# Kernel tuning notes

Measured on AMD Instinct MI355X. Metric: run time of the kernel, lower is better.

## Reference

```python
import jax, jax.numpy as jnp
import numpy as np
import math

# Static multi-level spatial layout (H, W) per level and flattened start offsets.
SHAPES = ((100, 100), (50, 50), (25, 25), (13, 13))
STARTS = (0, 10000, 12500, 13125)
LEN_IN = 13294
D_MODEL, N_LEVELS, N_HEADS, N_POINTS = 256, 4, 8, 4
D_HEAD = D_MODEL // N_HEADS
B, LQ = 2, 13294


def _offset_bias():
    # Replicates MSDeformAttn._reset_parameters radial grid init for sampling_offsets.bias
    thetas = np.arange(N_HEADS, dtype=np.float32) * (2.0 * math.pi / N_HEADS)
    grid = np.stack([np.cos(thetas), np.sin(thetas)], axis=-1)  # [nh, 2]
    grid = grid / np.abs(grid).max(axis=-1, keepdims=True)
    # [nh, nl, np, 2] with per-point radius (i+1)
    full = np.tile(grid[:, None, None, :], (1, N_LEVELS, N_POINTS, 1))
    full = full * np.arange(1, N_POINTS + 1, dtype=np.float32)[None, None, :, None]
    return full.reshape(-1)


def setup_inputs() -> dict:
    key = jax.random.key(0)
    ks = jax.random.split(key, 8)
    xavier = 1.0 / math.sqrt(D_MODEL)
    return {
        "query": jax.random.normal(ks[0], (B, LQ, D_MODEL), jnp.float32),
        "reference_points": jax.random.uniform(ks[1], (B, LQ, N_LEVELS, 2), jnp.float32),
        "input_flatten": jax.random.normal(ks[2], (B, LEN_IN, D_MODEL), jnp.float32),
        "input_spatial_shapes": jnp.array(SHAPES, jnp.int32),
        "input_level_start_index": jnp.array(STARTS, jnp.int32),
        "W_off": jax.random.normal(ks[3], (D_MODEL, N_HEADS * N_LEVELS * N_POINTS * 2), jnp.float32) * 0.01,
        "b_off": jnp.asarray(_offset_bias()),
        "W_attn": jax.random.normal(ks[4], (D_MODEL, N_HEADS * N_LEVELS * N_POINTS), jnp.float32) * 0.02,
        "b_attn": jnp.zeros((N_HEADS * N_LEVELS * N_POINTS,), jnp.float32),
        "W_val": jax.random.normal(ks[5], (D_MODEL, D_MODEL), jnp.float32) * xavier,
        "b_val": jnp.zeros((D_MODEL,), jnp.float32),
        "W_out": jax.random.normal(ks[6], (D_MODEL, D_MODEL), jnp.float32) * xavier,
        "b_out": jnp.zeros((D_MODEL,), jnp.float32),
    }


def reference(query, reference_points, input_flatten, input_spatial_shapes,
              input_level_start_index, W_off, b_off, W_attn, b_attn,
              W_val, b_val, W_out, b_out):
    Bq, Lq, _ = query.shape
    value = (input_flatten @ W_val + b_val).reshape(Bq, LEN_IN, N_HEADS, D_HEAD)

    off = (query @ W_off + b_off).reshape(Bq, Lq, N_HEADS, N_LEVELS, N_POINTS, 2)
    aw = (query @ W_attn + b_attn).reshape(Bq, Lq, N_HEADS, N_LEVELS * N_POINTS)
    aw = jax.nn.softmax(aw, axis=-1).reshape(Bq, Lq, N_HEADS, N_LEVELS, N_POINTS)

    # offset normalizer is (W, H) per level
    normalizer = jnp.array([[w, h] for (h, w) in SHAPES], query.dtype)  # [nl, 2]
    loc = reference_points[:, :, None, :, None, :] + off / normalizer[None, None, None, :, None, :]

    bi = jnp.arange(Bq)[:, None, None, None]
    hi = jnp.arange(N_HEADS)[None, None, :, None]
    out = jnp.zeros((Bq, Lq, N_HEADS, D_HEAD), query.dtype)

    # Per-level zero-padded bilinear sampling (math-equivalent to grid_sample
    # align_corners=False, padding_mode='zeros' on the padded max_H x max_W grid,
    # since the padded region is zero-filled).
    for lvl, (H, W) in enumerate(SHAPES):
        s = STARTS[lvl]
        vflat = value[:, s:s + H * W]  # [B, H*W, nh, dh]
        l = loc[:, :, :, lvl]          # [B, Lq, nh, P, 2] in normalized coords
        x = l[..., 0] * W - 0.5
        y = l[..., 1] * H - 0.5
        x0 = jnp.floor(x)
        y0 = jnp.floor(y)
        sampled = jnp.zeros((Bq, Lq, N_HEADS, N_POINTS, D_HEAD), query.dtype)
        for dx in (0, 1):
            for dy in (0, 1):
                xi = x0 + dx
                yi = y0 + dy
                wgt = (1.0 - jnp.abs(x - xi)) * (1.0 - jnp.abs(y - yi))
                valid = (xi >= 0) & (xi <= W - 1) & (yi >= 0) & (yi <= H - 1)
                idx = (jnp.clip(yi, 0, H - 1) * W + jnp.clip(xi, 0, W - 1)).astype(jnp.int32)
                v = vflat[bi, idx, hi]  # [B, Lq, nh, P, dh]
                sampled = sampled + v * (wgt * valid)[..., None]
        out = out + jnp.einsum('bqhpd,bqhp->bqhd', sampled, aw[:, :, :, lvl])

    out = out.reshape(Bq, Lq, D_MODEL)
    return out @ W_out + b_out
```

## Files before the change

kernel.cpp:

```cpp
#include <hip/hip_runtime.h>
#include <math.h>

#define BQ 2
#define LQ 13294
#define LEN_IN 13294
#define D_MODEL 256
#define N_HEADS 8
#define N_LEVELS 4
#define N_POINTS 4
#define D_HEAD 32
#define M_ROWS (BQ * LQ)

__device__ __constant__ int c_HW[N_LEVELS]    = {100, 50, 25, 13};
__device__ __constant__ int c_START[N_LEVELS] = {0, 10000, 12500, 13125};

typedef __attribute__((ext_vector_type(8))) short bf16x8;
typedef __attribute__((ext_vector_type(4))) float f32x4;

__device__ inline unsigned short f2bf(float f) {
  union { float f; unsigned int u; } x; x.f = f;
  unsigned int u = x.u;
  unsigned int r = (u + 0x7fffu + ((u >> 16) & 1u)) >> 16;
  return (unsigned short)r;
}
__device__ inline float bf2f(unsigned short b) {
  union { unsigned int u; float f; } x; x.u = ((unsigned int)b) << 16;
  return x.f;
}

__global__ __launch_bounds__(256) void prep_weights(
    const float* __restrict__ W_off, const float* __restrict__ b_off,
    const float* __restrict__ W_attn, const float* __restrict__ b_attn,
    const float* __restrict__ W_val, const float* __restrict__ W_out,
    unsigned short* __restrict__ Wval_t, unsigned short* __restrict__ Woa_t,
    unsigned short* __restrict__ Wout_t, float* __restrict__ b_oa) {
  const int idx = blockIdx.x * 256 + threadIdx.x;
  const int SZ1 = 256 * 256;
  const int SZ2 = 384 * 256;
  if (idx < SZ1) {
    const int n = idx >> 8, k = idx & 255;
    Wval_t[idx] = f2bf(W_val[k * 256 + n]);
  } else if (idx < SZ1 + SZ2) {
    const int j = idx - SZ1;
    const int n = j >> 8, k = j & 255;
    const float v = (n < 256) ? W_off[k * 256 + n] : W_attn[k * 128 + (n - 256)];
    Woa_t[j] = f2bf(v);
  } else if (idx < SZ1 + SZ2 + SZ1) {
    const int j = idx - SZ1 - SZ2;
    const int n = j >> 8, k = j & 255;
    Wout_t[j] = f2bf(W_out[k * 256 + n]);
  }
  if (blockIdx.x == 0) b_oa[threadIdx.x] = b_off[threadIdx.x];
  if (blockIdx.x == 1 && threadIdx.x < 128)
    b_oa[256 + threadIdx.x] = b_attn[threadIdx.x];
}

#define BM 128
#define BN 128
#define BK 32
#define LDK 40

template <bool A_BF16, bool C_BF16>
__global__ __launch_bounds__(256) void gemm_mfma(
    const void* __restrict__ Ap, const unsigned short* __restrict__ Wt,
    const float* __restrict__ bias, void* __restrict__ Cp,
    int M, int N, int K) {
  __shared__ unsigned short As[BM * LDK];
  __shared__ unsigned short Bs[BN * LDK];
  const int tid = threadIdx.x;
  const int m0 = blockIdx.x * BM;
  const int n0 = blockIdx.y * BN;
  const int wave = tid >> 6;
  const int lane = tid & 63;
  const int wm = (wave & 1) * 64;
  const int wn = (wave >> 1) * 64;
  const int fr = lane & 15;
  const int fq = lane >> 4;

  f32x4 acc[4][4];
#pragma unroll
  for (int i = 0; i < 4; ++i)
#pragma unroll
    for (int j = 0; j < 4; ++j) acc[i][j] = (f32x4){0.f, 0.f, 0.f, 0.f};

  for (int k0 = 0; k0 < K; k0 += BK) {
    if (A_BF16) {
      const int m = tid >> 2;
      const int ch = tid & 3;
#pragma unroll
      for (int half = 0; half < 2; ++half) {
        const int mm = m + half * 64;
        const int gm = m0 + mm;
        uint4 v = make_uint4(0u, 0u, 0u, 0u);
        if (gm < M)
          v = *(const uint4*)((const unsigned short*)Ap + (size_t)gm * K + k0 + ch * 8);
        *(uint4*)&As[mm * LDK + ch * 8] = v;
      }
    } else {
      const int m = tid >> 3;
      const int kq = tid & 7;
#pragma unroll
      for (int qtr = 0; qtr < 4; ++qtr) {
        const int mm = m + qtr * 32;
        const int gm = m0 + mm;
        float4 v = make_float4(0.f, 0.f, 0.f, 0.f);
        if (gm < M)
          v = *(const float4*)((const float*)Ap + (size_t)gm * K + k0 + kq * 4);
        ushort4 h;
        h.x = f2bf(v.x); h.y = f2bf(v.y); h.z = f2bf(v.z); h.w = f2bf(v.w);
        *(ushort4*)&As[mm * LDK + kq * 4] = h;
      }
    }
    {
      const int n = tid >> 2;
      const int ch = tid & 3;
#pragma unroll
      for (int half = 0; half < 2; ++half) {
        const int nn = n + half * 64;
        uint4 v = *(const uint4*)(Wt + (size_t)(n0 + nn) * K + k0 + ch * 8);
        *(uint4*)&Bs[nn * LDK + ch * 8] = v;
      }
    }
    __syncthreads();

    bf16x8 af[4], bfr[4];
#pragma unroll
    for (int i = 0; i < 4; ++i)
      af[i] = *(const bf16x8*)&As[(wm + i * 16 + fr) * LDK + fq * 8];
#pragma unroll
    for (int j = 0; j < 4; ++j)
      bfr[j] = *(const bf16x8*)&Bs[(wn + j * 16 + fr) * LDK + fq * 8];
#pragma unroll
    for (int i = 0; i < 4; ++i)
#pragma unroll
      for (int j = 0; j < 4; ++j)
        acc[i][j] = __builtin_amdgcn_mfma_f32_16x16x32_bf16(af[i], bfr[j],
                                                            acc[i][j], 0, 0, 0);
    __syncthreads();
  }

  const int col = fr;
  const int row0 = fq * 4;
#pragma unroll
  for (int i = 0; i < 4; ++i) {
#pragma unroll
    for (int j = 0; j < 4; ++j) {
      const int gn = n0 + wn + j * 16 + col;
      const float bb = bias[gn];
#pragma unroll
      for (int r = 0; r < 4; ++r) {
        const int gm = m0 + wm + i * 16 + row0 + r;
        if (gm < M) {
          const float v = acc[i][j][r] + bb;
          if (C_BF16)
            ((unsigned short*)Cp)[(size_t)gm * N + gn] = f2bf(v);
          else
            ((float*)Cp)[(size_t)gm * N + gn] = v;
        }
      }
    }
  }
}

__global__ __launch_bounds__(256) void sample_kernel(
    const float* __restrict__ refp,
    const float* __restrict__ oa,
    const unsigned short* __restrict__ value,
    unsigned int* __restrict__ mid) {
  const int tid = threadIdx.x;
  const int qi = tid >> 7;
  const int q = blockIdx.x * 2 + qi;
  const int b = (q >= LQ) ? 1 : 0;

  __shared__ float2 s_wo[2][4][136];

  {
    const int pid = tid & 127;
    const int h = pid >> 4;
    const int lp = pid & 15;
    const int l = lp >> 2;
    const int p = lp & 3;
    const int HW = c_HW[l];
    const float fW = (float)HW;

    const float logit = oa[(size_t)q * 384 + 256 + pid];
    float mx = logit;
#pragma unroll
    for (int s = 1; s < 16; s <<= 1) mx = fmaxf(mx, __shfl_xor(mx, s, 16));
    float e = expf(logit - mx);
    float sum = e;
#pragma unroll
    for (int s = 1; s < 16; s <<= 1) sum += __shfl_xor(sum, s, 16);
    const float a = e / sum;

    const float2 o = *(const float2*)&oa[(size_t)q * 384 + h * 32 + l * 8 + p * 2];
    const float rx = refp[((size_t)q * 4 + l) * 2 + 0];
    const float ry = refp[((size_t)q * 4 + l) * 2 + 1];
    const float x = (rx + o.x / fW) * fW - 0.5f;
    const float y = (ry + o.y / fW) * fW - 0.5f;
    const float x0 = floorf(x);
    const float y0 = floorf(y);

#pragma unroll
    for (int t = 0; t < 4; ++t) {
      const int dx = t & 1;
      const int dy = t >> 1;
      const float xi = x0 + (float)dx;
      const float yi = y0 + (float)dy;
      const float wgt = (1.0f - fabsf(x - xi)) * (1.0f - fabsf(y - yi));
      const bool valid =
          (xi >= 0.f) && (xi <= fW - 1.f) && (yi >= 0.f) && (yi <= fW - 1.f);
      int xc = (int)xi; xc = xc < 0 ? 0 : (xc > HW - 1 ? HW - 1 : xc);
      int yc = (int)yi; yc = yc < 0 ? 0 : (yc > HW - 1 ? HW - 1 : yc);
      const int row = b * LEN_IN + c_START[l] + yc * HW + xc;
      const int byteoff = row * 512 + h * 64;
      float2 wo;
      wo.x = valid ? wgt * a : 0.f;
      wo.y = __int_as_float(byteoff);
      s_wo[qi][t][pid + h] = wo;
    }
  }
  __syncthreads();

  {
    const int g = tid & 127;
    const int h = g >> 4;
    const int dp = g & 15;
    const char* vbase = (const char*)value + dp * 4;
    float acc0 = 0.f, acc1 = 0.f;
#pragma unroll 4
    for (int lp = 0; lp < 16; ++lp) {
      const int si = h * 16 + lp + h;
#pragma unroll
      for (int t = 0; t < 4; ++t) {
        const float2 f = s_wo[qi][t][si];
        const int off = __float_as_int(f.y);
        const unsigned int v = *(const unsigned int*)(vbase + off);
        acc0 += f.x * __uint_as_float(v << 16);
        acc1 += f.x * __uint_as_float(v & 0xffff0000u);
      }
    }
    const unsigned int packed =
        (unsigned int)f2bf(acc0) | ((unsigned int)f2bf(acc1) << 16);
    mid[(size_t)q * 128 + h * 16 + dp] = packed;
  }
}

extern "C" void kernel_launch(void* const* d_in, const int* in_sizes, int n_in,
                              void* d_out, int out_size, void* d_ws,
                              size_t ws_size, hipStream_t stream) {
  const float* query  = (const float*)d_in[0];
  const float* refp   = (const float*)d_in[1];
  const float* inpf   = (const float*)d_in[2];
  const float* W_off  = (const float*)d_in[5];
  const float* b_off  = (const float*)d_in[6];
  const float* W_attn = (const float*)d_in[7];
  const float* b_attn = (const float*)d_in[8];
  const float* W_val  = (const float*)d_in[9];
  const float* b_val  = (const float*)d_in[10];
  const float* W_out  = (const float*)d_in[11];
  const float* b_out  = (const float*)d_in[12];
  float* out = (float*)d_out;

  unsigned char* w = (unsigned char*)d_ws;
  unsigned short* Wval_t = (unsigned short*)w;            w += 256 * 256 * 2;
  unsigned short* Woa_t  = (unsigned short*)w;            w += 384 * 256 * 2;
  unsigned short* Wout_t = (unsigned short*)w;            w += 256 * 256 * 2;
  float*          b_oa   = (float*)w;                     w += 384 * 4 + 64;
  unsigned short* v_buf  = (unsigned short*)w;            w += (size_t)M_ROWS * 256 * 2;
  float*          oa_buf = (float*)w;                     w += (size_t)M_ROWS * 384 * 4;
  unsigned int*   mid_buf = (unsigned int*)w;

  const dim3 blk(256);
  const int mg = (M_ROWS + BM - 1) / BM;

  prep_weights<<<dim3(896), blk, 0, stream>>>(W_off, b_off, W_attn, b_attn,
                                              W_val, W_out, Wval_t, Woa_t,
                                              Wout_t, b_oa);
  gemm_mfma<false, true><<<dim3(mg, 2), blk, 0, stream>>>(
      inpf, Wval_t, b_val, v_buf, M_ROWS, 256, 256);
  gemm_mfma<false, false><<<dim3(mg, 3), blk, 0, stream>>>(
      query, Woa_t, b_oa, oa_buf, M_ROWS, 384, 256);
  sample_kernel<<<dim3(M_ROWS / 2), blk, 0, stream>>>(refp, oa_buf, v_buf,
                                                      mid_buf);
  gemm_mfma<true, false><<<dim3(mg, 2), blk, 0, stream>>>(
      mid_buf, Wout_t, b_out, out, M_ROWS, 256, 256);
}
```

Measured before the change: 235.7 us.

## Pre-convert inputs to bf16, use direct-to-LDS swizzled GEMM loads, fp16 offsets, wider sampling

Adds a conversion pass that casts query and input_flatten to bf16 ahead of the GEMMs. The GEMM now loads tiles with global_load_lds into XOR-swizzled LDS at BK=64, replacing register staging with padded rows. The offset/attention GEMM writes fp16 instead of fp32, which halves that intermediate's traffic but costs some precision. The sampling kernel handles four queries per block and gathers 8-byte vectors per lane, so each load carries four channels. The extra conversion pass adds a full read and write of both inputs in exchange for cheaper GEMM loads.

Measured after the change: 223.8 us. 5.0% less time.

```diff
diff --git a/kernel.cpp b/kernel.cpp
--- a/kernel.cpp
+++ b/kernel.cpp
@@ -4,37 +4,60 @@
 #define BQ 2
 #define LQ 13294
 #define LEN_IN 13294
-#define D_MODEL 256
-#define N_HEADS 8
-#define N_LEVELS 4
-#define N_POINTS 4
-#define D_HEAD 32
-#define M_ROWS (BQ * LQ)
-
-__device__ __constant__ int c_HW[N_LEVELS]    = {100, 50, 25, 13};
-__device__ __constant__ int c_START[N_LEVELS] = {0, 10000, 12500, 13125};
+#define M_ROWS 26588
+
+__device__ __constant__ int c_HW[4]    = {100, 50, 25, 13};
+__device__ __constant__ int c_START[4] = {0, 10000, 12500, 13125};
 
 typedef __attribute__((ext_vector_type(8))) short bf16x8;
 typedef __attribute__((ext_vector_type(4))) float f32x4;
+typedef __attribute__((ext_vector_type(2))) float f32x2;
 
 __device__ inline unsigned short f2bf(float f) {
   union { float f; unsigned int u; } x; x.f = f;
   unsigned int u = x.u;
-  unsigned int r = (u + 0x7fffu + ((u >> 16) & 1u)) >> 16;
-  return (unsigned short)r;
-}
-__device__ inline float bf2f(unsigned short b) {
-  union { unsigned int u; float f; } x; x.u = ((unsigned int)b) << 16;
-  return x.f;
-}
-
-__global__ __launch_bounds__(256) void prep_weights(
+  return (unsigned short)((u + 0x7fffu + ((u >> 16) & 1u)) >> 16);
+}
+__device__ inline float h2f(unsigned short h) {
+  _Float16 x; __builtin_memcpy(&x, &h, 2); return (float)x;
+}
+__device__ inline unsigned short f2h(float f) {
+  _Float16 x = (_Float16)f; unsigned short u; __builtin_memcpy(&u, &x, 2); return u;
+}
+
+__device__ inline void gl_lds16(const void* g, void* l) {
+  __builtin_amdgcn_global_load_lds(
+      (const __attribute__((address_space(1))) unsigned int*)g,
+      (__attribute__((address_space(3))) unsigned int*)l, 16, 0, 0);
+}
+
+#define CONV_BLKS 3456
+#define N4EACH (M_ROWS * 64)
+
+__global__ __launch_bounds__(256) void prep_all(
+    const float* __restrict__ query, const float* __restrict__ inpf,
     const float* __restrict__ W_off, const float* __restrict__ b_off,
     const float* __restrict__ W_attn, const float* __restrict__ b_attn,
     const float* __restrict__ W_val, const float* __restrict__ W_out,
+    unsigned short* __restrict__ q_bf, unsigned short* __restrict__ in_bf,
     unsigned short* __restrict__ Wval_t, unsigned short* __restrict__ Woa_t,
     unsigned short* __restrict__ Wout_t, float* __restrict__ b_oa) {
-  const int idx = blockIdx.x * 256 + threadIdx.x;
+  const int bx = blockIdx.x;
+  if (bx < CONV_BLKS) {
+    int i = bx * 256 + threadIdx.x;
+    const int stride = CONV_BLKS * 256;
+    for (; i < 2 * N4EACH; i += stride) {
+      const float* src; unsigned short* dst; int j;
+      if (i < N4EACH) { src = query; dst = q_bf; j = i; }
+      else            { src = inpf;  dst = in_bf; j = i - N4EACH; }
+      const float4 v = ((const float4*)src)[j];
+      ushort4 h;
+      h.x = f2bf(v.x); h.y = f2bf(v.y); h.z = f2bf(v.z); h.w = f2bf(v.w);
+      ((ushort4*)dst)[j] = h;
+    }
+    return;
+  }
+  const int idx = (bx - CONV_BLKS) * 256 + threadIdx.x;
   const int SZ1 = 256 * 256;
   const int SZ2 = 384 * 256;
   if (idx < SZ1) {
@@ -45,37 +68,43 @@
     const int n = j >> 8, k = j & 255;
     const float v = (n < 256) ? W_off[k * 256 + n] : W_attn[k * 128 + (n - 256)];
     Woa_t[j] = f2bf(v);
-  } else if (idx < SZ1 + SZ2 + SZ1) {
+  } else {
     const int j = idx - SZ1 - SZ2;
     const int n = j >> 8, k = j & 255;
     Wout_t[j] = f2bf(W_out[k * 256 + n]);
   }
-  if (blockIdx.x == 0) b_oa[threadIdx.x] = b_off[threadIdx.x];
-  if (blockIdx.x == 1 && threadIdx.x < 128)
+  if (bx == CONV_BLKS) b_oa[threadIdx.x] = b_off[threadIdx.x];
+  if (bx == CONV_BLKS + 1 && threadIdx.x < 128)
     b_oa[256 + threadIdx.x] = b_attn[threadIdx.x];
 }
 
-#define BM 128
-#define BN 128
-#define BK 32
-#define LDK 40
-
-template <bool A_BF16, bool C_BF16>
+template <int CT>
 __global__ __launch_bounds__(256) void gemm_mfma(
-    const void* __restrict__ Ap, const unsigned short* __restrict__ Wt,
-    const float* __restrict__ bias, void* __restrict__ Cp,
-    int M, int N, int K) {
-  __shared__ unsigned short As[BM * LDK];
-  __shared__ unsigned short Bs[BN * LDK];
+    const unsigned short* __restrict__ A, const unsigned short* __restrict__ Wt,
+    const float* __restrict__ bias, void* __restrict__ Cp, int M, int N) {
+  __shared__ unsigned short As[128 * 64];
+  __shared__ unsigned short Bs[128 * 64];
   const int tid = threadIdx.x;
-  const int m0 = blockIdx.x * BM;
-  const int n0 = blockIdx.y * BN;
-  const int wave = tid >> 6;
+  const int wv = tid >> 6;
   const int lane = tid & 63;
-  const int wm = (wave & 1) * 64;
-  const int wn = (wave >> 1) * 64;
+  const int m0 = blockIdx.x * 128;
+  const int n0 = blockIdx.y * 128;
+  const int wm = (wv & 1) * 64;
+  const int wn = (wv >> 1) * 64;
   const int fr = lane & 15;
   const int fq = lane >> 4;
+  const int lr = lane >> 3;
+  const int gch = (lane & 7) ^ lr;
+
+  const unsigned short* ga[4];
+  const unsigned short* gb[4];
+#pragma unroll
+  for (int t = 0; t < 4; ++t) {
+    int ar = m0 + wv * 32 + t * 8 + lr;
+    if (ar > M - 1) ar = M - 1;
+    ga[t] = A + (size_t)ar * 256 + gch * 8;
+    gb[t] = Wt + (size_t)(n0 + wv * 32 + t * 8 + lr) * 256 + gch * 8;
+  }
 
   f32x4 acc[4][4];
 #pragma unroll
@@ -83,60 +112,35 @@
 #pragma unroll
     for (int j = 0; j < 4; ++j) acc[i][j] = (f32x4){0.f, 0.f, 0.f, 0.f};
 
-  for (int k0 = 0; k0 < K; k0 += BK) {
-    if (A_BF16) {
-      const int m = tid >> 2;
-      const int ch = tid & 3;
-#pragma unroll
-      for (int half = 0; half < 2; ++half) {
-        const int mm = m + half * 64;
-        const int gm = m0 + mm;
-        uint4 v = make_uint4(0u, 0u, 0u, 0u);
-        if (gm < M)
-          v = *(const uint4*)((const unsigned short*)Ap + (size_t)gm * K + k0 + ch * 8);
-        *(uint4*)&As[mm * LDK + ch * 8] = v;
-      }
-    } else {
-      const int m = tid >> 3;
-      const int kq = tid & 7;
-#pragma unroll
-      for (int qtr = 0; qtr < 4; ++qtr) {
-        const int mm = m + qtr * 32;
-        const int gm = m0 + mm;
-        float4 v = make_float4(0.f, 0.f, 0.f, 0.f);
-        if (gm < M)
-          v = *(const float4*)((const float*)Ap + (size_t)gm * K + k0 + kq * 4);
-        ushort4 h;
-        h.x = f2bf(v.x); h.y = f2bf(v.y); h.z = f2bf(v.z); h.w = f2bf(v.w);
-        *(ushort4*)&As[mm * LDK + kq * 4] = h;
-      }
-    }
-    {
-      const int n = tid >> 2;
-      const int ch = tid & 3;
-#pragma unroll
-      for (int half = 0; half < 2; ++half) {
-        const int nn = n + half * 64;
-        uint4 v = *(const uint4*)(Wt + (size_t)(n0 + nn) * K + k0 + ch * 8);
-        *(uint4*)&Bs[nn * LDK + ch * 8] = v;
-      }
-    }
+  for (int k0 = 0; k0 < 256; k0 += 64) {
     __syncthreads();
-
-    bf16x8 af[4], bfr[4];
-#pragma unroll
-    for (int i = 0; i < 4; ++i)
-      af[i] = *(const bf16x8*)&As[(wm + i * 16 + fr) * LDK + fq * 8];
-#pragma unroll
-    for (int j = 0; j < 4; ++j)
-      bfr[j] = *(const bf16x8*)&Bs[(wn + j * 16 + fr) * LDK + fq * 8];
-#pragma unroll
-    for (int i = 0; i < 4; ++i)
-#pragma unroll
-      for (int j = 0; j < 4; ++j)
-        acc[i][j] = __builtin_amdgcn_mfma_f32_16x16x32_bf16(af[i], bfr[j],
-                                                            acc[i][j], 0, 0, 0);
+#pragma unroll
+    for (int t = 0; t < 4; ++t) {
+      gl_lds16(ga[t], &As[(wv * 32 + t * 8) * 64]);
+      gl_lds16(gb[t], &Bs[(wv * 32 + t * 8) * 64]);
+      ga[t] += 64; gb[t] += 64;
+    }
     __syncthreads();
+#pragma unroll
+    for (int kk = 0; kk < 2; ++kk) {
+      bf16x8 af[4], bf[4];
+#pragma unroll
+      for (int i = 0; i < 4; ++i) {
+        const int row = wm + i * 16 + fr;
+        af[i] = *(const bf16x8*)&As[row * 64 + ((kk * 4 + fq) ^ (row & 7)) * 8];
+      }
+#pragma unroll
+      for (int j = 0; j < 4; ++j) {
+        const int row = wn + j * 16 + fr;
+        bf[j] = *(const bf16x8*)&Bs[row * 64 + ((kk * 4 + fq) ^ (row & 7)) * 8];
+      }
+#pragma unroll
+      for (int i = 0; i < 4; ++i)
+#pragma unroll
+        for (int j = 0; j < 4; ++j)
+          acc[i][j] = __builtin_amdgcn_mfma_f32_16x16x32_bf16(af[i], bf[j],
+                                                              acc[i][j], 0, 0, 0);
+    }
   }
 
   const int col = fr;
@@ -152,8 +156,10 @@
         const int gm = m0 + wm + i * 16 + row0 + r;
         if (gm < M) {
           const float v = acc[i][j][r] + bb;
-          if (C_BF16)
+          if (CT == 1)
             ((unsigned short*)Cp)[(size_t)gm * N + gn] = f2bf(v);
+          else if (CT == 2)
+            ((unsigned short*)Cp)[(size_t)gm * N + gn] = f2h(v);
           else
             ((float*)Cp)[(size_t)gm * N + gn] = v;
         }
@@ -164,15 +170,13 @@
 
 __global__ __launch_bounds__(256) void sample_kernel(
     const float* __restrict__ refp,
-    const float* __restrict__ oa,
+    const unsigned short* __restrict__ oa,
     const unsigned short* __restrict__ value,
     unsigned int* __restrict__ mid) {
   const int tid = threadIdx.x;
-  const int qi = tid >> 7;
-  const int q = blockIdx.x * 2 + qi;
-  const int b = (q >= LQ) ? 1 : 0;
-
-  __shared__ float2 s_wo[2][4][136];
+  const int q0 = blockIdx.x * 4;
+
+  __shared__ float2 s_wo[4][4][136];
 
   {
     const int pid = tid & 127;
@@ -182,67 +186,82 @@
     const int p = lp & 3;
     const int HW = c_HW[l];
     const float fW = (float)HW;
-
-    const float logit = oa[(size_t)q * 384 + 256 + pid];
-    float mx = logit;
-#pragma unroll
-    for (int s = 1; s < 16; s <<= 1) mx = fmaxf(mx, __shfl_xor(mx, s, 16));
-    float e = expf(logit - mx);
-    float sum = e;
-#pragma unroll
-    for (int s = 1; s < 16; s <<= 1) sum += __shfl_xor(sum, s, 16);
-    const float a = e / sum;
-
-    const float2 o = *(const float2*)&oa[(size_t)q * 384 + h * 32 + l * 8 + p * 2];
-    const float rx = refp[((size_t)q * 4 + l) * 2 + 0];
-    const float ry = refp[((size_t)q * 4 + l) * 2 + 1];
-    const float x = (rx + o.x / fW) * fW - 0.5f;
-    const float y = (ry + o.y / fW) * fW - 0.5f;
-    const float x0 = floorf(x);
-    const float y0 = floorf(y);
-
-#pragma unroll
-    for (int t = 0; t < 4; ++t) {
-      const int dx = t & 1;
-      const int dy = t >> 1;
-      const float xi = x0 + (float)dx;
-      const float yi = y0 + (float)dy;
-      const float wgt = (1.0f - fabsf(x - xi)) * (1.0f - fabsf(y - yi));
-      const bool valid =
-          (xi >= 0.f) && (xi <= fW - 1.f) && (yi >= 0.f) && (yi <= fW - 1.f);
-      int xc = (int)xi; xc = xc < 0 ? 0 : (xc > HW - 1 ? HW - 1 : xc);
-      int yc = (int)yi; yc = yc < 0 ? 0 : (yc > HW - 1 ? HW - 1 : yc);
-      const int row = b * LEN_IN + c_START[l] + yc * HW + xc;
-      const int byteoff = row * 512 + h * 64;
-      float2 wo;
-      wo.x = valid ? wgt * a : 0.f;
-      wo.y = __int_as_float(byteoff);
-      s_wo[qi][t][pid + h] = wo;
+    const int sub = tid >> 7;
+#pragma unroll
+    for (int qq = 0; qq < 2; ++qq) {
+      const int qi = sub * 2 + qq;
+      const int q = q0 + qi;
+      const int b = (q >= LQ) ? 1 : 0;
+
+      const float logit = h2f(oa[(size_t)q * 384 + 256 + pid]);
+      float mx = logit;
+#pragma unroll
+      for (int s = 1; s < 16; s <<= 1) mx = fmaxf(mx, __shfl_xor(mx, s, 16));
+      const float e = expf(logit - mx);
+      float sum = e;
+#pragma unroll
+      for (int s = 1; s < 16; s <<= 1) sum += __shfl_xor(sum, s, 16);
+      const float a = e / sum;
+
+      const unsigned int opk =
+          *(const unsigned int*)&oa[(size_t)q * 384 + h * 32 + l * 8 + p * 2];
+      const float ox = h2f((unsigned short)(opk & 0xffffu));
+      const float oy = h2f((unsigned short)(opk >> 16));
+      const float rx = refp[((size_t)q * 4 + l) * 2 + 0];
+      const float ry = refp[((size_t)q * 4 + l) * 2 + 1];
+      const float x = (rx + ox / fW) * fW - 0.5f;
+      const float y = (ry + oy / fW) * fW - 0.5f;
+      const float x0 = floorf(x);
+      const float y0 = floorf(y);
+
+#pragma unroll
+      for (int t = 0; t < 4; ++t) {
+        const int dx = t & 1;
+        const int dy = t >> 1;
+        const float xi = x0 + (float)dx;
+        const float yi = y0 + (float)dy;
+        const float wgt = (1.0f - fabsf(x - xi)) * (1.0f - fabsf(y - yi));
+        const bool valid =
+            (xi >= 0.f) && (xi <= fW - 1.f) && (yi >= 0.f) && (yi <= fW - 1.f);
+        int xc = (int)xi; xc = xc < 0 ? 0 : (xc > HW - 1 ? HW - 1 : xc);
+        int yc = (int)yi; yc = yc < 0 ? 0 : (yc > HW - 1 ? HW - 1 : yc);
+        const int row = b * LEN_IN + c_START[l] + yc * HW + xc;
+        float2 wo;
+        wo.x = valid ? wgt * a : 0.f;
+        wo.y = __int_as_float(row * 512 + h * 64);
+        s_wo[qi][t][h * 17 + lp] = wo;
+      }
     }
   }
   __syncthreads();
 
   {
-    const int g = tid & 127;
-    const int h = g >> 4;
-    const int dp = g & 15;
-    const char* vbase = (const char*)value + dp * 4;
-    float acc0 = 0.f, acc1 = 0.f;
+    const int qi = tid >> 6;
+    const int g = tid & 63;
+    const int h = g >> 3;
+    const int dp8 = g & 7;
+    const int q = q0 + qi;
+    const char* vbase = (const char*)value + dp8 * 8;
+    f32x2 acc0 = {0.f, 0.f}, acc1 = {0.f, 0.f};
 #pragma unroll 4
     for (int lp = 0; lp < 16; ++lp) {
-      const int si = h * 16 + lp + h;
+      const int si = h * 17 + lp;
 #pragma unroll
       for (int t = 0; t < 4; ++t) {
         const float2 f = s_wo[qi][t][si];
-        const int off = __float_as_int(f.y);
-        const unsigned int v = *(const unsigned int*)(vbase + off);
-        acc0 += f.x * __uint_as_float(v << 16);
-        acc1 += f.x * __uint_as_float(v & 0xffff0000u);
-      }
-    }
-    const unsigned int packed =
-        (unsigned int)f2bf(acc0) | ((unsigned int)f2bf(acc1) << 16);
-    mid[(size_t)q * 128 + h * 16 + dp] = packed;
+        const uint2 v = *(const uint2*)(vbase + __float_as_int(f.y));
+        f32x2 av0 = {__uint_as_float(v.x << 16),
+                     __uint_as_float(v.x & 0xffff0000u)};
+        f32x2 av1 = {__uint_as_float(v.y << 16),
+                     __uint_as_float(v.y & 0xffff0000u)};
+        acc0 += f.x * av0;
+        acc1 += f.x * av1;
+      }
+    }
+    uint2 pk;
+    pk.x = (unsigned int)f2bf(acc0.x) | ((unsigned int)f2bf(acc0.y) << 16);
+    pk.y = (unsigned int)f2bf(acc1.x) | ((unsigned int)f2bf(acc1.y) << 16);
+    *(uint2*)&mid[(size_t)q * 128 + h * 16 + dp8 * 2] = pk;
   }
 }
 
@@ -263,26 +282,28 @@
   float* out = (float*)d_out;
 
   unsigned char* w = (unsigned char*)d_ws;
-  unsigned short* Wval_t = (unsigned short*)w;            w += 256 * 256 * 2;
-  unsigned short* Woa_t  = (unsigned short*)w;            w += 384 * 256 * 2;
-  unsigned short* Wout_t = (unsigned short*)w;            w += 256 * 256 * 2;
-  float*          b_oa   = (float*)w;                     w += 384 * 4 + 64;
-  unsigned short* v_buf  = (unsigned short*)w;            w += (size_t)M_ROWS * 256 * 2;
-  float*          oa_buf = (float*)w;                     w += (size_t)M_ROWS * 384 * 4;
+  unsigned short* Wval_t = (unsigned short*)w;  w += 256 * 256 * 2;
+  unsigned short* Woa_t  = (unsigned short*)w;  w += 384 * 256 * 2;
+  unsigned short* Wout_t = (unsigned short*)w;  w += 256 * 256 * 2;
+  float*          b_oa   = (float*)w;           w += 384 * 4 + 64;
+  unsigned short* q_bf   = (unsigned short*)w;  w += (size_t)M_ROWS * 256 * 2;
+  unsigned short* in_bf  = (unsigned short*)w;  w += (size_t)M_ROWS * 256 * 2;
+  unsigned short* v_buf  = (unsigned short*)w;  w += (size_t)M_ROWS * 256 * 2;
+  unsigned short* oa_buf = (unsigned short*)w;  w += (size_t)M_ROWS * 384 * 2;
   unsigned int*   mid_buf = (unsigned int*)w;
 
   const dim3 blk(256);
-  const int mg = (M_ROWS + BM - 1) / BM;
-
-  prep_weights<<<dim3(896), blk, 0, stream>>>(W_off, b_off, W_attn, b_attn,
-                                              W_val, W_out, Wval_t, Woa_t,
-                                              Wout_t, b_oa);
-  gemm_mfma<false, true><<<dim3(mg, 2), blk, 0, stream>>>(
-      inpf, Wval_t, b_val, v_buf, M_ROWS, 256, 256);
-  gemm_mfma<false, false><<<dim3(mg, 3), blk, 0, stream>>>(
-      query, Woa_t, b_oa, oa_buf, M_ROWS, 384, 256);
-  sample_kernel<<<dim3(M_ROWS / 2), blk, 0, stream>>>(refp, oa_buf, v_buf,
+  const int mg = (M_ROWS + 127) / 128;
+
+  prep_all<<<dim3(CONV_BLKS + 896), blk, 0, stream>>>(
+      query, inpf, W_off, b_off, W_attn, b_attn, W_val, W_out,
+      q_bf, in_bf, Wval_t, Woa_t, Wout_t, b_oa);
+  gemm_mfma<1><<<dim3(mg, 2), blk, 0, stream>>>(in_bf, Wval_t, b_val, v_buf,
+                                                M_ROWS, 256);
+  gemm_mfma<2><<<dim3(mg, 3), blk, 0, stream>>>(q_bf, Woa_t, b_oa, oa_buf,
+                                                M_ROWS, 384);
+  sample_kernel<<<dim3(M_ROWS / 4), blk, 0, stream>>>(refp, oa_buf, v_buf,
                                                       mid_buf);
-  gemm_mfma<true, false><<<dim3(mg, 2), blk, 0, stream>>>(
-      mid_buf, Wout_t, b_out, out, M_ROWS, 256, 256);
-}
+  gemm_mfma<0><<<dim3(mg, 2), blk, 0, stream>>>((const unsigned short*)mid_buf,
+                                                Wout_t, b_out, out, M_ROWS, 256);
+}
```
